# Optimization experiments

Hardware: AMD Instinct MI355X
Metric: run time of the kernel (lower is better)

Reference implementation:

```python
import jax, jax.numpy as jnp
import numpy as np

MODES = 32
WIDTH = 64
FACTOR = 2
N_LAYERS = 4


def dct_matrix(N):
    # Ortho DCT-II matrix D: dct(x) along last axis = x @ D.T ; idct(y) = y @ D
    n = jnp.arange(N, dtype=jnp.float32)
    k = n[:, None]
    D = jnp.cos(jnp.pi * (n[None, :] + 0.5) * k / N) * jnp.sqrt(2.0 / N)
    D = D.at[0].mul(1.0 / jnp.sqrt(2.0))
    return D


def setup_inputs() -> dict:
    key = jax.random.key(0)
    ks = jax.random.split(key, 16)
    B, M, N, IN_DIM = 4, 256, 256, 12
    hid = WIDTH * FACTOR
    xav_f = jnp.sqrt(2.0 / (WIDTH + WIDTH))  # xavier_normal for (in,out,modes)
    inp = {
        'x': jax.random.normal(ks[0], (B, M, N, IN_DIM), jnp.float32),
        'W_in': jax.random.normal(ks[1], (WIDTH, IN_DIM), jnp.float32) * (1.0 / jnp.sqrt(IN_DIM)),
        'b_in': jnp.zeros((WIDTH,), jnp.float32),
        'fw0': jax.random.normal(ks[2], (N_LAYERS, WIDTH, WIDTH, MODES), jnp.float32) * xav_f,
        'fw1': jax.random.normal(ks[3], (N_LAYERS, WIDTH, WIDTH, MODES), jnp.float32) * xav_f,
        'ffW1': jax.random.normal(ks[4], (N_LAYERS, hid, WIDTH), jnp.float32) * (1.0 / jnp.sqrt(WIDTH)),
        'ffb1': jnp.zeros((N_LAYERS, hid), jnp.float32),
        'ffW2': jax.random.normal(ks[5], (N_LAYERS, WIDTH, hid), jnp.float32) * (1.0 / jnp.sqrt(hid)),
        'ffb2': jnp.zeros((N_LAYERS, WIDTH), jnp.float32),
        'W_o1': jax.random.normal(ks[6], (128, WIDTH), jnp.float32) * (1.0 / jnp.sqrt(WIDTH)),
        'b_o1': jnp.zeros((128,), jnp.float32),
        'W_o2': jax.random.normal(ks[7], (1, 128), jnp.float32) * (1.0 / jnp.sqrt(128.0)),
        'b_o2': jnp.zeros((1,), jnp.float32),
    }
    return inp


def forward_fourier(x, w0, w1, DM, DN):
    # x: [B, M, N, I] channels-last -> [B, I, M, N]
    x = jnp.transpose(x, (0, 3, 1, 2))
    # --- y direction: DCT along N, truncated mode mix, IDCT ---
    x_fty = jnp.einsum('bimn,kn->bimk', x, DN)            # dct, [B,I,M,N]
    xy_m = jnp.einsum('bixy,ioy->boxy', x_fty[..., :MODES], w0)  # [B,O,M,modes]
    xy = jnp.einsum('boxy,yn->boxn', xy_m, DN[:MODES, :])        # idct of zero-padded spectrum
    # --- x direction: DCT along M ---
    x2 = jnp.swapaxes(x, -1, -2)                          # [B,I,N,M]
    x_ftx = jnp.einsum('binm,km->bink', x2, DM)
    xx_m = jnp.einsum('bixy,ioy->boxy', x_ftx[..., :MODES], w1)  # [B,O,N,modes]
    xx = jnp.einsum('boxy,ym->boxm', xx_m, DM[:MODES, :])        # [B,O,N,M]
    xx = jnp.swapaxes(xx, -1, -2)                         # [B,O,M,N]
    out = xx + xy
    return jnp.transpose(out, (0, 2, 3, 1))               # [B,M,N,O]


def feed_forward(h, W1, b1, W2, b2):
    h = jax.nn.relu(h @ W1.T + b1)
    return h @ W2.T + b2


def reference(x, W_in, b_in, fw0, fw1, ffW1, ffb1, ffW2, ffb2, W_o1, b_o1, W_o2, b_o2):
    B, M, N, _ = x.shape
    DM = dct_matrix(M)
    DN = dct_matrix(N)
    x = x @ W_in.T + b_in                                  # in_proj, [B,M,N,width]
    b = x
    for i in range(N_LAYERS):
        h = forward_fourier(x, fw0[i], fw1[i], DM, DN)
        b = feed_forward(h, ffW1[i], ffb1[i], ffW2[i], ffb2[i])
        x = x + b
    # use_fork=False: out applied to the LAST backcast b
    o = jax.nn.relu(b @ W_o1.T + b_o1) * 0 + (b @ W_o1.T + b_o1)  # WNLinear has no activation
    o = b @ W_o1.T + b_o1
    forecast = o @ W_o2.T + b_o2                           # [B,M,N,1]
    return forecast
```

## Files before the change

kernel.cpp:

```cpp
#include <hip/hip_runtime.h>
#include <hip/hip_bf16.h>
#include <math.h>

#define BATCH 4
#define MMDIM 256
#define NNDIM 256
#define CH 64
#define NMODES 32
#define HID 128
#define NLAYERS 4
#define XPLANE 16777216L

typedef __attribute__((ext_vector_type(8))) short bfrag;
typedef __attribute__((ext_vector_type(8))) ushort u16x8;
typedef __attribute__((ext_vector_type(4))) float f32x4;

__device__ inline ushort f2bf(float x) {
    union { float f; uint u; } v; v.f = x;
    uint r = v.u + 0x7fff + ((v.u >> 16) & 1);
    return (ushort)(r >> 16);
}
__device__ inline float bf2f(ushort h) {
    union { uint u; float f; } v; v.u = (uint)h << 16; return v.f;
}
__device__ inline void split(float v, ushort& hi, ushort& lo) {
    __hip_bfloat16 h = __float2bfloat16(v);
    hi = __builtin_bit_cast(ushort, h);
    lo = __builtin_bit_cast(ushort, __float2bfloat16(v - __bfloat162float(h)));
}
#define MFMA __builtin_amdgcn_mfma_f32_16x16x32_bf16


__global__ __launch_bounds__(256) void k_Tfrag(ushort* __restrict__ Tf) {
    int idx = blockIdx.x * 256 + threadIdx.x;
    int j = idx & 7, lane = (idx >> 3) & 63, ks = (idx >> 9) & 7, yt = idx >> 12;
    int k = yt * 16 + (lane & 15);
    int n = ks * 32 + ((lane >> 4) << 3) + j;
    double v = cos(M_PI * (n + 0.5) * (double)k / 256.0) * 0.08838834764831845;
    if (k == 0) v *= 0.7071067811865476;
    float vf = (float)v;
    ushort hh = f2bf(vf);
    Tf[idx] = hh; Tf[idx + 8192] = f2bf(vf - bf2f(hh));
}

__global__ __launch_bounds__(256) void k_Ttfrag(ushort* __restrict__ Ttf) {
    int idx = blockIdx.x * 256 + threadIdx.x;
    int j = idx & 7, lane = (idx >> 3) & 63, at = idx >> 9;
    int k = ((lane >> 4) << 3) + j;
    int n = at * 16 + (lane & 15);
    double v = cos(M_PI * (n + 0.5) * (double)k / 256.0) * 0.08838834764831845;
    if (k == 0) v *= 0.7071067811865476;
    float vf = (float)v;
    ushort hh = f2bf(vf);
    Ttf[idx] = hh; Ttf[idx + 8192] = f2bf(vf - bf2f(hh));
}

__global__ __launch_bounds__(256) void k_wt(const float* __restrict__ fw0, const float* __restrict__ fw1,
                                            float* __restrict__ wt01) {
    int idx = blockIdx.x * 256 + threadIdx.x;
    const float* fw = (idx < 524288) ? fw0 : fw1;
    int i2 = idx & 524287;
    int l = i2 >> 17, r = i2 & 131071;
    int y = r >> 12, i = (r >> 6) & 63, o = r & 63;
    wt01[idx] = fw[((l * 64 + i) * 64 + o) * 32 + y];
}

__global__ __launch_bounds__(256) void k_wfrag(const float* __restrict__ W,
                                               ushort* __restrict__ hi, ushort* __restrict__ lo,
                                               int N, int K) {
    int idx = blockIdx.x * 256 + threadIdx.x;
    int per_l = N * K;
    int l = idx / per_l, r = idx % per_l;
    int jj = r & 7, lane = (r >> 3) & 63;
    int ks = (r >> 9) % (K >> 5);
    int nt = r / (512 * (K >> 5));
    int row = nt * 16 + (lane & 15);
    int col = ks * 32 + ((lane >> 4) << 3) + jj;
    float v = W[(long)l * per_l + row * K + col];
    ushort h = f2bf(v);
    hi[idx] = h;
    lo[idx] = f2bf(v - bf2f(h));
}

__global__ void k_head(const float* __restrict__ W_o1, const float* __restrict__ b_o1,
                       const float* __restrict__ W_o2, const float* __restrict__ b_o2,
                       float* __restrict__ Weff, float* __restrict__ beff) {
    int c = threadIdx.x;
    float acc = 0.f;
    for (int j = 0; j < 128; j++) acc += W_o2[j] * W_o1[j * 64 + c];
    Weff[c] = acc;
    if (c == 0) {
        float bb = 0.f;
        for (int j = 0; j < 128; j++) bb += W_o2[j] * b_o1[j];
        beff[0] = bb + b_o2[0];
    }
}

__global__ __launch_bounds__(256) void k_inproj_bf(const float* __restrict__ xin,
                                                   const float* __restrict__ W_in,
                                                   const float* __restrict__ b_in,
                                                   ushort* __restrict__ xbf) {
    __shared__ __align__(16) ushort tile[2][64][72];
    int t = threadIdx.x;
    int bid = blockIdx.x;
    int b = bid >> 10, m = (bid >> 2) & 255, n0 = (bid & 3) * 64;
    int c = t & 63, ng = t >> 6;
    long pbase = (long)(b * 256 + m) * 256 + n0;
    float w[12];
#pragma unroll
    for (int d = 0; d < 12; d++) w[d] = W_in[c * 12 + d];
    float bc = b_in[c];
#pragma unroll 4
    for (int i = 0; i < 16; i++) {
        int nl = ng * 16 + i;
        const float* xr = xin + (pbase + nl) * 12;
        float acc = bc;
#pragma unroll
        for (int d = 0; d < 12; d++) acc += xr[d] * w[d];
        ushort hh, ll;
        split(acc, hh, ll);
        tile[0][c][nl] = hh;
        tile[1][c][nl] = ll;
    }
    __syncthreads();
    int c2 = t >> 2, ch = t & 3;
#pragma unroll
    for (int pl = 0; pl < 2; pl++) {
        const ushort* s = &tile[pl][c2][ch * 16];
        u16x8 v0 = *(const u16x8*)s;
        u16x8 v1 = *(const u16x8*)(s + 8);
        ushort* dst = xbf + (long)pl * XPLANE + ((long)(b * 256 + m) * 64 + c2) * 256 + n0 + ch * 16;
        *(u16x8*)dst = v0; *(u16x8*)(dst + 8) = v1;
    }
}

__global__ __launch_bounds__(256) void k_tx(const ushort* __restrict__ src, ushort* __restrict__ dst) {
    __shared__ __align__(16) ushort tl[64][72];
    int t = threadIdx.x;
    int bid = blockIdx.x;
    int ntile = bid & 3, mt = (bid >> 2) & 3, c = (bid >> 4) & 63, b = (bid >> 10) & 3, pl = bid >> 12;
    int m0 = mt * 64, n0 = ntile * 64;
    const ushort* sp = src + (long)pl * XPLANE;
    ushort* dp = dst + (long)pl * XPLANE;
    {
        int row = t >> 2, ch = (t & 3) * 16;
        const ushort* p = sp + ((long)(b * 256 + m0 + row) * 64 + c) * 256 + n0 + ch;
        u16x8 v0 = *(const u16x8*)p;
        u16x8 v1 = *(const u16x8*)(p + 8);
#pragma unroll
        for (int k = 0; k < 8; k++) tl[ch + k][row] = v0[k];
#pragma unroll
        for (int k = 0; k < 8; k++) tl[ch + 8 + k][row] = v1[k];
    }
    __syncthreads();
    {
        int nrow = t >> 2, mch = (t & 3) * 16;
        const ushort* s = &tl[nrow][mch];
        u16x8 v0 = *(const u16x8*)s;
        u16x8 v1 = *(const u16x8*)(s + 8);
        ushort* p = dp + ((long)(b * 256 + n0 + nrow) * 64 + c) * 256 + m0 + mch;
        *(u16x8*)p = v0; *(u16x8*)(p + 8) = v1;
    }
}

__global__ __launch_bounds__(512) void k_spec(const ushort* __restrict__ xbf,
                                              const ushort* __restrict__ Tf,
                                              const ushort* __restrict__ Ttf,
                                              const float* __restrict__ wt,
                                              float* __restrict__ hdst,
                                              long strideA, long strideF, int accum) {
    __shared__ float Xs[2][32][68];
    __shared__ __align__(16) ushort Xmb[2][2][64][40];
    int t = threadIdx.x;
    int lane = t & 63, wv = t >> 6, l15 = lane & 15, l4 = lane >> 4;
    int fp = blockIdx.x & 127, b = blockIdx.x >> 7;
    int s_ = wv >> 2;

    {
        const ushort* xb = xbf + ((long)(b * 256 + fp * 2 + s_)) * 16384;
        f32x4 a0 = {0.f, 0.f, 0.f, 0.f}, a1 = {0.f, 0.f, 0.f, 0.f};
        int c0 = (wv & 3) * 16;
#pragma unroll
        for (int ks = 0; ks < 8; ks++) {
            const ushort* bp = xb + (c0 + l15) * 256 + ks * 32 + l4 * 8;
            bfrag bhi = *(const bfrag*)bp;
            bfrag blo = *(const bfrag*)(bp + XPLANE);
            const ushort* ap0 = Tf + (long)((0 * 8 + ks) * 64 + lane) * 8;
            const ushort* ap1 = Tf + (long)((1 * 8 + ks) * 64 + lane) * 8;
            bfrag a0h = *(const bfrag*)ap0, a0l = *(const bfrag*)(ap0 + 8192);
            bfrag a1h = *(const bfrag*)ap1, a1l = *(const bfrag*)(ap1 + 8192);
            a0 = MFMA(a0h, bhi, a0, 0, 0, 0);
            a0 = MFMA(a0h, blo, a0, 0, 0, 0);
            a0 = MFMA(a0l, bhi, a0, 0, 0, 0);
            a1 = MFMA(a1h, bhi, a1, 0, 0, 0);
            a1 = MFMA(a1h, blo, a1, 0, 0, 0);
            a1 = MFMA(a1l, bhi, a1, 0, 0, 0);
        }
#pragma unroll
        for (int r = 0; r < 4; r++) {
            Xs[s_][l4 * 4 + r][c0 + l15] = a0[r];
            Xs[s_][16 + l4 * 4 + r][c0 + l15] = a1[r];
        }
    }
    __syncthreads();

    {
        int og = t & 15, y = t >> 4;
        const float* wb = wt + (long)y * 4096 + og * 4;
        f32x4 A0 = {0.f, 0.f, 0.f, 0.f}, A1 = {0.f, 0.f, 0.f, 0.f};
#pragma unroll 8
        for (int i = 0; i < 64; i++) {
            float4 wv4 = *(const float4*)(wb + i * 64);
            float x0 = Xs[0][y][i];
            float x1 = Xs[1][y][i];
            A0.x += x0 * wv4.x; A0.y += x0 * wv4.y; A0.z += x0 * wv4.z; A0.w += x0 * wv4.w;
            A1.x += x1 * wv4.x; A1.y += x1 * wv4.y; A1.z += x1 * wv4.z; A1.w += x1 * wv4.w;
        }
#pragma unroll
        for (int e = 0; e < 4; e++) {
            ushort hh, ll;
            split(A0[e], hh, ll);
            Xmb[0][0][og * 4 + e][y] = hh;
            Xmb[0][1][og * 4 + e][y] = ll;
            split(A1[e], hh, ll);
            Xmb[1][0][og * 4 + e][y] = hh;
            Xmb[1][1][og * 4 + e][y] = ll;
        }
    }
    __syncthreads();

    bfrag vbh[4], vbl[4];
#pragma unroll
    for (int ot = 0; ot < 4; ot++) {
        vbh[ot] = *(const bfrag*)(&Xmb[s_][0][ot * 16 + l15][l4 * 8]);
        vbl[ot] = *(const bfrag*)(&Xmb[s_][1][ot * 16 + l15][l4 * 8]);
    }
    int f = fp * 2 + s_;
    float* hb = hdst + (long)b * 4194304 + (long)f * strideF;
#pragma unroll
    for (int ai = 0; ai < 4; ai++) {
        int at = (wv & 3) * 4 + ai;
        const ushort* ap = Ttf + (long)(at * 64 + lane) * 8;
        bfrag th = *(const bfrag*)ap, tl_ = *(const bfrag*)(ap + 8192);
#pragma unroll
        for (int ot = 0; ot < 4; ot++) {
            f32x4 acc = {0.f, 0.f, 0.f, 0.f};
            acc = MFMA(th, vbh[ot], acc, 0, 0, 0);
            acc = MFMA(th, vbl[ot], acc, 0, 0, 0);
            acc = MFMA(tl_, vbh[ot], acc, 0, 0, 0);
            int arow = at * 16 + l4 * 4;
            float* op = hb + (long)arow * strideA + ot * 16 + l15;
            if (accum) {
#pragma unroll
                for (int r = 0; r < 4; r++) op[(long)r * strideA] += acc[r];
            } else {
#pragma unroll
                for (int r = 0; r < 4; r++) op[(long)r * strideA] = acc[r];
            }
        }
    }
}

#define ASW 136
__global__ __launch_bounds__(256) void k_ff(const float* __restrict__ h,
                                            ushort* __restrict__ xbfw,
                                            const ushort* __restrict__ W1hi, const ushort* __restrict__ W1lo,
                                            const float* __restrict__ b1,
                                            const ushort* __restrict__ W2hi, const ushort* __restrict__ W2lo,
                                            const float* __restrict__ b2,
                                            const float* __restrict__ Weff, const float* __restrict__ beff,
                                            float* __restrict__ out, int last) {
    __shared__ __align__(16) ushort Asb[2][64][ASW];
    int t = threadIdx.x;
    int lane = t & 63, wv = t >> 6;
    int l15 = lane & 15, l4 = lane >> 4;
    long p0 = (long)blockIdx.x * 64;

    f32x4 acc1[8];
#pragma unroll
    for (int nt = 0; nt < 8; nt++) acc1[nt] = (f32x4){0.f, 0.f, 0.f, 0.f};
#pragma unroll
    for (int ks = 0; ks < 2; ks++) {
        const float* hp = h + (p0 + wv * 16 + l15) * 64 + ks * 32 + l4 * 8;
        float4 h0 = *(const float4*)hp;
        float4 h1 = *(const float4*)(hp + 4);
        bfrag ahi, alo;
#pragma unroll
        for (int j = 0; j < 8; j++) {
            float v = (j < 4) ? (&h0.x)[j] : (&h1.x)[j - 4];
            ushort hh, ll;
            split(v, hh, ll);
            ahi[j] = (short)hh; alo[j] = (short)ll;
        }
#pragma unroll
        for (int nt = 0; nt < 8; nt++) {
            long off = (long)((nt * 2 + ks) * 64 + lane) * 8;
            bfrag bhi = *(const bfrag*)(W1hi + off);
            bfrag blo = *(const bfrag*)(W1lo + off);
            acc1[nt] = MFMA(ahi, bhi, acc1[nt], 0, 0, 0);
            acc1[nt] = MFMA(ahi, blo, acc1[nt], 0, 0, 0);
            acc1[nt] = MFMA(alo, bhi, acc1[nt], 0, 0, 0);
        }
    }
#pragma unroll
    for (int nt = 0; nt < 8; nt++) {
        float bj = b1[nt * 16 + l15];
        int j = nt * 16 + l15;
#pragma unroll
        for (int r = 0; r < 4; r++) {
            float v = fmaxf(acc1[nt][r] + bj, 0.f);
            int px = wv * 16 + l4 * 4 + r;
            ushort hh, ll;
            split(v, hh, ll);
            Asb[0][px][j] = hh;
            Asb[1][px][j] = ll;
        }
    }
    __syncthreads();

    f32x4 acc2[4];
#pragma unroll
    for (int nt = 0; nt < 4; nt++) acc2[nt] = (f32x4){0.f, 0.f, 0.f, 0.f};
#pragma unroll
    for (int ks = 0; ks < 4; ks++) {
        bfrag ahi = *(const bfrag*)(&Asb[0][wv * 16 + l15][ks * 32 + l4 * 8]);
        bfrag alo = *(const bfrag*)(&Asb[1][wv * 16 + l15][ks * 32 + l4 * 8]);
#pragma unroll
        for (int nt = 0; nt < 4; nt++) {
            long off = (long)((nt * 4 + ks) * 64 + lane) * 8;
            bfrag bhi = *(const bfrag*)(W2hi + off);
            bfrag blo = *(const bfrag*)(W2lo + off);
            acc2[nt] = MFMA(ahi, bhi, acc2[nt], 0, 0, 0);
            acc2[nt] = MFMA(ahi, blo, acc2[nt], 0, 0, 0);
            acc2[nt] = MFMA(alo, bhi, acc2[nt], 0, 0, 0);
        }
    }

    if (last) {
        float be = beff[0];
#pragma unroll
        for (int r = 0; r < 4; r++) {
            float v = 0.f;
#pragma unroll
            for (int nt = 0; nt < 4; nt++) {
                int c = nt * 16 + l15;
                v += (acc2[nt][r] + b2[c]) * Weff[c];
            }
            v += __shfl_xor(v, 1, 64);
            v += __shfl_xor(v, 2, 64);
            v += __shfl_xor(v, 4, 64);
            v += __shfl_xor(v, 8, 64);
            if (l15 == 0) out[p0 + wv * 16 + l4 * 4 + r] = v + be;
        }
    } else {
        __syncthreads();
        ushort* tile = &Asb[0][0][0];
        int b = (int)(p0 >> 16), m = (int)((p0 >> 8) & 255), n0 = (int)(p0 & 255);
        int c2 = t >> 2, ch = t & 3;
#pragma unroll
        for (int pl = 0; pl < 2; pl++) {
            const ushort* src = xbfw + (long)pl * XPLANE + ((long)(b * 256 + m) * 64 + c2) * 256 + n0 + ch * 16;
            u16x8 v0 = *(const u16x8*)src;
            u16x8 v1 = *(const u16x8*)(src + 8);
            ushort* d = tile + (pl * 64 + c2) * 72 + ch * 16;
            *(u16x8*)d = v0; *(u16x8*)(d + 8) = v1;
        }
        __syncthreads();
#pragma unroll
        for (int nt = 0; nt < 4; nt++) {
            int c = nt * 16 + l15;
            float bc = b2[c];
#pragma unroll
            for (int r = 0; r < 4; r++) {
                int nl = wv * 16 + l4 * 4 + r;
                float res = bf2f(tile[(0 * 64 + c) * 72 + nl]) + bf2f(tile[(1 * 64 + c) * 72 + nl]);
                float v = res + acc2[nt][r] + bc;
                ushort hh, ll;
                split(v, hh, ll);
                tile[(0 * 64 + c) * 72 + nl] = hh;
                tile[(1 * 64 + c) * 72 + nl] = ll;
            }
        }
        __syncthreads();
#pragma unroll
        for (int pl = 0; pl < 2; pl++) {
            const ushort* s = tile + (pl * 64 + c2) * 72 + ch * 16;
            u16x8 v0 = *(const u16x8*)s;
            u16x8 v1 = *(const u16x8*)(s + 8);
            ushort* dst = xbfw + (long)pl * XPLANE + ((long)(b * 256 + m) * 64 + c2) * 256 + n0 + ch * 16;
            *(u16x8*)dst = v0; *(u16x8*)(dst + 8) = v1;
        }
    }
}


extern "C" void kernel_launch(void* const* d_in, const int* in_sizes, int n_in,
                              void* d_out, int out_size, void* d_ws, size_t ws_size,
                              hipStream_t stream) {
    const float* x_in = (const float*)d_in[0];
    const float* W_in = (const float*)d_in[1];
    const float* b_in = (const float*)d_in[2];
    const float* fw0  = (const float*)d_in[3];
    const float* fw1  = (const float*)d_in[4];
    const float* ffW1 = (const float*)d_in[5];
    const float* ffb1 = (const float*)d_in[6];
    const float* ffW2 = (const float*)d_in[7];
    const float* ffb2 = (const float*)d_in[8];
    const float* W_o1 = (const float*)d_in[9];
    const float* b_o1 = (const float*)d_in[10];
    const float* W_o2 = (const float*)d_in[11];
    const float* b_o2 = (const float*)d_in[12];
    float* out = (float*)d_out;

    float* ws   = (float*)d_ws;
    float* w0t  = ws;
    float* w1t  = w0t + 524288;
    float* Weff = w1t + 524288;
    float* beff = Weff + 64;
    float* h    = beff + 64;
    ushort* Tfrag  = (ushort*)(h + 16777216);
    ushort* Ttfrag = Tfrag + 16384;
    ushort* W1f_hi = Ttfrag + 16384;
    ushort* W1f_lo = W1f_hi + 32768;
    ushort* W2f_hi = W1f_lo + 32768;
    ushort* W2f_lo = W2f_hi + 32768;
    ushort* xbf_y  = W2f_lo + 32768;
    ushort* xbf_x  = xbf_y + 2 * XPLANE;

    k_Tfrag<<<32, 256, 0, stream>>>(Tfrag);
    k_Ttfrag<<<32, 256, 0, stream>>>(Ttfrag);
    k_wt<<<4096, 256, 0, stream>>>(fw0, fw1, w0t);
    k_wfrag<<<(NLAYERS * HID * CH) / 256, 256, 0, stream>>>(ffW1, W1f_hi, W1f_lo, HID, CH);
    k_wfrag<<<(NLAYERS * CH * HID) / 256, 256, 0, stream>>>(ffW2, W2f_hi, W2f_lo, CH, HID);
    k_head<<<1, 64, 0, stream>>>(W_o1, b_o1, W_o2, b_o2, Weff, beff);
    k_inproj_bf<<<4096, 256, 0, stream>>>(x_in, W_in, b_in, xbf_y);

    for (int l = 0; l < NLAYERS; l++) {
        k_spec<<<512, 512, 0, stream>>>(xbf_y, Tfrag, Ttfrag, w0t + (long)l * 131072,
                                        h, 64L, 16384L, 0);
        k_tx<<<8192, 256, 0, stream>>>(xbf_y, xbf_x);
        k_spec<<<512, 512, 0, stream>>>(xbf_x, Tfrag, Ttfrag, w1t + (long)l * 131072,
                                        h, 16384L, 64L, 1);
        k_ff<<<4096, 256, 0, stream>>>(h, xbf_y,
            W1f_hi + (long)l * HID * CH, W1f_lo + (long)l * HID * CH,
            ffb1 + (long)l * HID,
            W2f_hi + (long)l * CH * HID, W2f_lo + (long)l * CH * HID,
            ffb2 + (long)l * CH,
            Weff, beff, out, (l == NLAYERS - 1) ? 1 : 0);
    }
}
```

Baseline: 675.5 us.

## Merge y and x spectral launches into one grid, write x-path as bf16

The two per-layer k_spec launches (y-direction and x-direction) become a single launch with twice the blocks, each block picking its path from its block index. The x-path writes its output to a separate bf16 buffer instead of doing a read-modify-write accumulate into the fp32 h buffer. k_ff then sums both buffers when it loads its input. This removes one launch and the serialising accumulate dependency, and halves the x-path write bytes. The cost is bf16 rounding of the x-path contribution (lower precision) plus an extra buffer read in k_ff.

```diff
diff --git a/kernel.cpp b/kernel.cpp
--- a/kernel.cpp
+++ b/kernel.cpp
@@ -27,6 +27,9 @@
     __hip_bfloat16 h = __float2bfloat16(v);
     hi = __builtin_bit_cast(ushort, h);
     lo = __builtin_bit_cast(ushort, __float2bfloat16(v - __bfloat162float(h)));
+}
+__device__ inline ushort f2bf_hw(float v) {
+    return __builtin_bit_cast(ushort, __float2bfloat16(v));
 }
 #define MFMA __builtin_amdgcn_mfma_f32_16x16x32_bf16
 
@@ -163,18 +166,25 @@
     }
 }
 
-__global__ __launch_bounds__(512) void k_spec(const ushort* __restrict__ xbf,
+__global__ __launch_bounds__(512) void k_spec(const ushort* __restrict__ xbf_y,
+                                              const ushort* __restrict__ xbf_x,
                                               const ushort* __restrict__ Tf,
                                               const ushort* __restrict__ Ttf,
-                                              const float* __restrict__ wt,
-                                              float* __restrict__ hdst,
-                                              long strideA, long strideF, int accum) {
+                                              const float* __restrict__ wt_y,
+                                              const float* __restrict__ wt_x,
+                                              float* __restrict__ hy,
+                                              ushort* __restrict__ hx) {
     __shared__ float Xs[2][32][68];
     __shared__ __align__(16) ushort Xmb[2][2][64][40];
     int t = threadIdx.x;
     int lane = t & 63, wv = t >> 6, l15 = lane & 15, l4 = lane >> 4;
-    int fp = blockIdx.x & 127, b = blockIdx.x >> 7;
+    int bid = blockIdx.x;
+    int xpath = bid >> 9;
+    int lb = bid & 511;
+    int fp = lb & 127, b = lb >> 7;
     int s_ = wv >> 2;
+    const ushort* xbf = xpath ? xbf_x : xbf_y;
+    const float* wt = xpath ? wt_x : wt_y;
 
     {
         const ushort* xb = xbf + ((long)(b * 256 + fp * 2 + s_)) * 16384;
@@ -236,7 +246,6 @@
         vbl[ot] = *(const bfrag*)(&Xmb[s_][1][ot * 16 + l15][l4 * 8]);
     }
     int f = fp * 2 + s_;
-    float* hb = hdst + (long)b * 4194304 + (long)f * strideF;
 #pragma unroll
     for (int ai = 0; ai < 4; ai++) {
         int at = (wv & 3) * 4 + ai;
@@ -249,20 +258,22 @@
             acc = MFMA(th, vbl[ot], acc, 0, 0, 0);
             acc = MFMA(tl_, vbh[ot], acc, 0, 0, 0);
             int arow = at * 16 + l4 * 4;
-            float* op = hb + (long)arow * strideA + ot * 16 + l15;
-            if (accum) {
-#pragma unroll
-                for (int r = 0; r < 4; r++) op[(long)r * strideA] += acc[r];
+            if (!xpath) {
+                float* op = hy + (long)b * 4194304 + (long)f * 16384 + (long)arow * 64 + ot * 16 + l15;
+#pragma unroll
+                for (int r = 0; r < 4; r++) op[r * 64] = acc[r];
             } else {
-#pragma unroll
-                for (int r = 0; r < 4; r++) op[(long)r * strideA] = acc[r];
+                ushort* op = hx + (long)b * 4194304 + (long)f * 64 + (long)arow * 16384 + ot * 16 + l15;
+#pragma unroll
+                for (int r = 0; r < 4; r++) op[(long)r * 16384] = f2bf_hw(acc[r]);
             }
         }
     }
 }
 
 #define ASW 136
-__global__ __launch_bounds__(256) void k_ff(const float* __restrict__ h,
+__global__ __launch_bounds__(256) void k_ff(const float* __restrict__ hy,
+                                            const ushort* __restrict__ hx,
                                             ushort* __restrict__ xbfw,
                                             const ushort* __restrict__ W1hi, const ushort* __restrict__ W1lo,
                                             const float* __restrict__ b1,
@@ -281,13 +292,15 @@
     for (int nt = 0; nt < 8; nt++) acc1[nt] = (f32x4){0.f, 0.f, 0.f, 0.f};
 #pragma unroll
     for (int ks = 0; ks < 2; ks++) {
-        const float* hp = h + (p0 + wv * 16 + l15) * 64 + ks * 32 + l4 * 8;
+        long boff = (p0 + wv * 16 + l15) * 64 + ks * 32 + l4 * 8;
+        const float* hp = hy + boff;
         float4 h0 = *(const float4*)hp;
         float4 h1 = *(const float4*)(hp + 4);
+        u16x8 hx8 = *(const u16x8*)(hx + boff);
         bfrag ahi, alo;
 #pragma unroll
         for (int j = 0; j < 8; j++) {
-            float v = (j < 4) ? (&h0.x)[j] : (&h1.x)[j - 4];
+            float v = ((j < 4) ? (&h0.x)[j] : (&h1.x)[j - 4]) + bf2f(hx8[j]);
             ushort hh, ll;
             split(v, hh, ll);
             ahi[j] = (short)hh; alo[j] = (short)ll;
@@ -417,8 +430,9 @@
     float* w1t  = w0t + 524288;
     float* Weff = w1t + 524288;
     float* beff = Weff + 64;
-    float* h    = beff + 64;
-    ushort* Tfrag  = (ushort*)(h + 16777216);
+    float* h_y  = beff + 64;
+    ushort* h_x = (ushort*)(h_y + 16777216);
+    ushort* Tfrag  = h_x + 16777216;
     ushort* Ttfrag = Tfrag + 16384;
     ushort* W1f_hi = Ttfrag + 16384;
     ushort* W1f_lo = W1f_hi + 32768;
@@ -436,12 +450,11 @@
     k_inproj_bf<<<4096, 256, 0, stream>>>(x_in, W_in, b_in, xbf_y);
 
     for (int l = 0; l < NLAYERS; l++) {
-        k_spec<<<512, 512, 0, stream>>>(xbf_y, Tfrag, Ttfrag, w0t + (long)l * 131072,
-                                        h, 64L, 16384L, 0);
         k_tx<<<8192, 256, 0, stream>>>(xbf_y, xbf_x);
-        k_spec<<<512, 512, 0, stream>>>(xbf_x, Tfrag, Ttfrag, w1t + (long)l * 131072,
-                                        h, 16384L, 64L, 1);
-        k_ff<<<4096, 256, 0, stream>>>(h, xbf_y,
+        k_spec<<<1024, 512, 0, stream>>>(xbf_y, xbf_x, Tfrag, Ttfrag,
+                                         w0t + (long)l * 131072, w1t + (long)l * 131072,
+                                         h_y, h_x);
+        k_ff<<<4096, 256, 0, stream>>>(h_y, h_x, xbf_y,
             W1f_hi + (long)l * HID * CH, W1f_lo + (long)l * HID * CH,
             ffb1 + (long)l * HID,
             W2f_hi + (long)l * CH * HID, W2f_lo + (long)l * CH * HID,
```

New measurement: 664.4 us. No clear change (-1.7%).
